# Kernel optimization log

Measured on AMD Instinct MI355X. Metric: run time of the kernel, lower is better.

## Reference

```python
import jax, jax.numpy as jnp
import numpy as np

ALPHA = 0.1  # leakyRNN default alpha


def setup_inputs() -> dict:
    key = jax.random.key(0)
    k1, k2, k3, k4 = jax.random.split(key, 4)
    B, T, N_in, n, N = 256, 2048, 3, 2, 128
    u = jax.random.normal(k1, (B, T, N_in), dtype=jnp.float32)
    matB = jax.random.uniform(k2, (N, N), dtype=jnp.float32)
    # scaled for recurrence stability over T=2048 steps (spectral radius of 0.9*I + 0.1*W < 1)
    wIn = jax.random.normal(k3, (n, N_in), dtype=jnp.float32) * 0.5
    wRec = jax.random.normal(k4, (n, n), dtype=jnp.float32) * 0.5
    return {"u": u, "matB": matB, "wIn": wIn, "wRec": wRec}


def reference(u, matB, wIn, wRec):
    B, T, _ = u.shape
    n = wRec.shape[0]
    N = matB.shape[0]

    # (bias=False, init_state_train=False -> y0 = 0)
    y0 = jnp.zeros((B, n), dtype=u.dtype)

    def step(y, xt):
        y = (1.0 - ALPHA) * y + ALPHA * (jax.nn.relu(y) @ wRec.T + xt @ wIn.T)
        return y, y

    _, hidden = jax.lax.scan(step, y0, jnp.swapaxes(u, 0, 1))  # [T,B,n]
    hidden = jnp.swapaxes(hidden, 0, 1)  # [B,T,n]

    # ZeroPad1d((0, N-n)) pads the last (feature) dim on the right
    x_padded = jnp.pad(hidden, ((0, 0), (0, 0), (0, N - n)))  # [B,T,N]

    # Orthonormal (Cayley) parametrization: A = B - B^T; Q solves Q @ (I+A) = (I-A)
    A = matB - matB.T
    I = jnp.eye(N, dtype=matB.dtype)
    Q = jnp.linalg.solve((I + A).T, (I - A).T).T  # (I-A) @ inv(I+A)

    # nn.Linear(N, N, bias=False) with weight Q: y = x @ Q^T
    return x_padded @ Q.T
```

## Files before the change

### kernel.cpp

```cpp
#include <hip/hip_runtime.h>

#define TT 2048
#define BATCH 256
#define LDC 132
#define NCOL 130

typedef float vfloat4 __attribute__((ext_vector_type(4)));


__global__ __launch_bounds__(256) void proj_kernel(
    const float* __restrict__ u, const float* __restrict__ wIn, float* __restrict__ ws)
{
    __shared__ float2 tile[64][33];
    const int tid = threadIdx.x;
    const int tb = blockIdx.x & 31;
    const int bb = blockIdx.x >> 5;
    const int t0 = tb * 64;
    const int b0 = bb * 32;

    const float w00 = 0.1f * wIn[0], w01 = 0.1f * wIn[1], w02 = 0.1f * wIn[2];
    const float w10 = 0.1f * wIn[3], w11 = 0.1f * wIn[4], w12 = 0.1f * wIn[5];

    const int tl  = tid & 63;
    const int bl0 = tid >> 6;
#pragma unroll
    for (int s = 0; s < 8; ++s) {
        int bl = bl0 + s * 4;
        const float* p = u + ((size_t)(b0 + bl) * TT + t0 + tl) * 3;
        float x = p[0], y = p[1], z = p[2];
        float2 dv;
        dv.x = fmaf(x, w00, fmaf(y, w01, z * w02));
        dv.y = fmaf(x, w10, fmaf(y, w11, z * w12));
        tile[tl][bl] = dv;
    }
    __syncthreads();

    float* d = ws + 256;
    const int bw  = tid & 31;
    const int tw0 = tid >> 5;
#pragma unroll
    for (int s = 0; s < 8; ++s) {
        int tw = tw0 + s * 8;
        *(float2*)(d + ((size_t)(t0 + tw) * BATCH + b0 + bw) * 2) = tile[tw][bw];
    }
}

__global__ __launch_bounds__(256) void ge_rnn_kernel(
    const float* __restrict__ matB, const float* __restrict__ wRec,
    float* __restrict__ ws)
{
    if (blockIdx.x == 0) {
        __shared__ __align__(16) float Mc[NCOL * LDC];
        __shared__ __align__(16) float fb[128];
        __shared__ float vb[256];
        const int tid = threadIdx.x;

        for (int e = tid; e < 128 * 128; e += 256) {
            int i = e >> 7, j = e & 127;
            float a = matB[i * 128 + j] - matB[j * 128 + i];
            Mc[j * LDC + i] = a + ((i == j) ? 1.0f : 0.0f);
        }
        for (int i = tid; i < 128; i += 256) {
            Mc[128 * LDC + i] = (i == 0) ? 1.0f : 0.0f;
            Mc[129 * LDC + i] = (i == 1) ? 1.0f : 0.0f;
        }
        __syncthreads();

        for (int k = 0; k < 127; ++k) {
            if (tid > k && tid < 128)
                fb[tid] = Mc[k * LDC + tid] / Mc[k * LDC + k];
            __syncthreads();
            int j = tid;
            if (j > k && j < NCOL) {
                float mkj = Mc[j * LDC + k];
                int i = k + 1;
                int iv = (i + 3) & ~3;
                if (iv > 128) iv = 128;
                for (; i < iv; ++i)
                    Mc[j * LDC + i] = fmaf(-fb[i], mkj, Mc[j * LDC + i]);
                for (; i < 128; i += 4) {
                    float4 m = *(float4*)&Mc[j * LDC + i];
                    float4 f = *(const float4*)&fb[i];
                    m.x = fmaf(-f.x, mkj, m.x);
                    m.y = fmaf(-f.y, mkj, m.y);
                    m.z = fmaf(-f.z, mkj, m.z);
                    m.w = fmaf(-f.w, mkj, m.w);
                    *(float4*)&Mc[j * LDC + i] = m;
                }
            }
            __syncthreads();
        }

        float r0 = 0.f, r1 = 0.f;
        if (tid < 128) {
            r0 = Mc[128 * LDC + tid];
            r1 = Mc[129 * LDC + tid];
        }
        for (int k = 127; k >= 0; --k) {
            if (tid == k) {
                float piv = Mc[k * LDC + k];
                vb[k]       = r0 / piv;
                vb[128 + k] = r1 / piv;
            }
            __syncthreads();
            if (tid < k) {
                float uik = Mc[k * LDC + tid];
                r0 = fmaf(-uik, vb[k],       r0);
                r1 = fmaf(-uik, vb[128 + k], r1);
            }
        }
        __syncthreads();

        if (tid < 128) {
            int i = tid;
            float q0 = vb[i], q1 = vb[128 + i];
            for (int j = 0; j < 128; ++j) {
                float aij = matB[i * 128 + j] - matB[j * 128 + i];
                q0 = fmaf(-aij, vb[j],       q0);
                q1 = fmaf(-aij, vb[128 + j], q1);
            }
            ws[i]       = q0;
            ws[128 + i] = q1;
        }
    } else if (blockIdx.x == 1) {
        const int b = threadIdx.x;
        float* dh = ws + 256;
        const float a00 = 0.1f * wRec[0], a01 = 0.1f * wRec[1];
        const float a10 = 0.1f * wRec[2], a11 = 0.1f * wRec[3];
        float y0 = 0.f, y1 = 0.f;

        const int G = 16;
        float2 cur[G], nxt[G];
#pragma unroll
        for (int k = 0; k < G; ++k)
            cur[k] = *(float2*)(dh + ((size_t)k * BATCH + b) * 2);

        for (int g = 0; g < TT / G; ++g) {
            if (g + 1 < TT / G) {
                int tn = (g + 1) * G;
#pragma unroll
                for (int k = 0; k < G; ++k)
                    nxt[k] = *(float2*)(dh + ((size_t)(tn + k) * BATCH + b) * 2);
            }
#pragma unroll
            for (int k = 0; k < G; ++k) {
                float rr0 = fmaxf(y0, 0.f), rr1 = fmaxf(y1, 0.f);
                float n0 = fmaf(rr0, a00, fmaf(rr1, a01, cur[k].x));
                float n1 = fmaf(rr0, a10, fmaf(rr1, a11, cur[k].y));
                y0 = fmaf(0.9f, y0, n0);
                y1 = fmaf(0.9f, y1, n1);
                cur[k].x = y0;
                cur[k].y = y1;
            }
#pragma unroll
            for (int k = 0; k < G; ++k)
                *(float2*)(dh + ((size_t)(g * G + k) * BATCH + b) * 2) = cur[k];
#pragma unroll
            for (int k = 0; k < G; ++k) cur[k] = nxt[k];
        }
    }
}

__global__ __launch_bounds__(256) void out_kernel(
    const float* __restrict__ ws, float* __restrict__ out)
{
    const int tid = threadIdx.x;
    const int jg  = tid & 31;
    const int sub = tid >> 5;
    float4 qa = *(const float4*)(ws + jg * 4);
    float4 qb = *(const float4*)(ws + 128 + jg * 4);
    const float* h = ws + 256;
    const int ngroups = BATCH * (TT / 8);
    for (int g = blockIdx.x; g < ngroups; g += gridDim.x) {
        int b = g >> 8;
        int t = (g & 255) * 8 + sub;
        float2 hv = *(const float2*)(h + ((size_t)t * BATCH + b) * 2);
        vfloat4 o;
        o.x = fmaf(hv.x, qa.x, hv.y * qb.x);
        o.y = fmaf(hv.x, qa.y, hv.y * qb.y);
        o.z = fmaf(hv.x, qa.z, hv.y * qb.z);
        o.w = fmaf(hv.x, qa.w, hv.y * qb.w);
        __builtin_nontemporal_store(o, (vfloat4*)(out + ((size_t)b * TT + t) * 128 + jg * 4));
    }
}

extern "C" void kernel_launch(void* const* d_in, const int* in_sizes, int n_in,
                              void* d_out, int out_size, void* d_ws, size_t ws_size,
                              hipStream_t stream) {
    const float* u    = (const float*)d_in[0];
    const float* matB = (const float*)d_in[1];
    const float* wIn  = (const float*)d_in[2];
    const float* wRec = (const float*)d_in[3];
    float* out = (float*)d_out;
    float* ws  = (float*)d_ws;

    hipLaunchKernelGGL(proj_kernel,   dim3(256),  dim3(256), 0, stream, u, wIn, ws);
    hipLaunchKernelGGL(ge_rnn_kernel, dim3(2),    dim3(256), 0, stream, matB, wRec, ws);
    hipLaunchKernelGGL(out_kernel,    dim3(8192), dim3(256), 0, stream, ws, out);
}
```

Before: 503.2 us.

## Split RNN across four blocks with t4-interleaved layout, L2 prefetch waves, and faster GE

Changes the workspace layout so each batch element owns a contiguous 8-float record per group of four timesteps. The recurrence now runs on four blocks of 64 lanes instead of one block of 256, with 16-byte loads in a double-buffered load/compute/store schedule. Three spare wavefronts per block read the block's slice ahead of time so it sits in cache. The Gaussian elimination also drops one barrier per pivot by computing the scale inline, and its back substitution now runs in a single wave using shuffles instead of barriers. The risk is the extra prefetch traffic and the added index arithmetic in out_kernel.

```diff
diff --git a/kernel.cpp b/kernel.cpp
--- a/kernel.cpp
+++ b/kernel.cpp
@@ -37,11 +37,20 @@
 
     float* d = ws + 256;
     const int bw  = tid & 31;
-    const int tw0 = tid >> 5;
-#pragma unroll
-    for (int s = 0; s < 8; ++s) {
-        int tw = tw0 + s * 8;
-        *(float2*)(d + ((size_t)(t0 + tw) * BATCH + b0 + bw) * 2) = tile[tw][bw];
+    const int tg0 = tid >> 5;
+#pragma unroll
+    for (int s = 0; s < 2; ++s) {
+        int t4l = tg0 + s * 8;
+        float2 a0 = tile[t4l * 4 + 0][bw];
+        float2 a1 = tile[t4l * 4 + 1][bw];
+        float2 a2 = tile[t4l * 4 + 2][bw];
+        float2 a3 = tile[t4l * 4 + 3][bw];
+        float* p = d + ((size_t)((t0 >> 2) + t4l) * BATCH + (b0 + bw)) * 8;
+        vfloat4 w0, w1;
+        w0.x = a0.x; w0.y = a0.y; w0.z = a1.x; w0.w = a1.y;
+        w1.x = a2.x; w1.y = a2.y; w1.z = a3.x; w1.w = a3.y;
+        *(vfloat4*)p       = w0;
+        *(vfloat4*)(p + 4) = w1;
     }
 }
 
@@ -51,7 +60,6 @@
 {
     if (blockIdx.x == 0) {
         __shared__ __align__(16) float Mc[NCOL * LDC];
-        __shared__ __align__(16) float fb[128];
         __shared__ float vb[256];
         const int tid = threadIdx.x;
 
@@ -67,46 +75,42 @@
         __syncthreads();
 
         for (int k = 0; k < 127; ++k) {
-            if (tid > k && tid < 128)
-                fb[tid] = Mc[k * LDC + tid] / Mc[k * LDC + k];
-            __syncthreads();
             int j = tid;
             if (j > k && j < NCOL) {
-                float mkj = Mc[j * LDC + k];
+                float scale = Mc[j * LDC + k] / Mc[k * LDC + k];
                 int i = k + 1;
                 int iv = (i + 3) & ~3;
                 if (iv > 128) iv = 128;
                 for (; i < iv; ++i)
-                    Mc[j * LDC + i] = fmaf(-fb[i], mkj, Mc[j * LDC + i]);
+                    Mc[j * LDC + i] = fmaf(-Mc[k * LDC + i], scale, Mc[j * LDC + i]);
                 for (; i < 128; i += 4) {
                     float4 m = *(float4*)&Mc[j * LDC + i];
-                    float4 f = *(const float4*)&fb[i];
-                    m.x = fmaf(-f.x, mkj, m.x);
-                    m.y = fmaf(-f.y, mkj, m.y);
-                    m.z = fmaf(-f.z, mkj, m.z);
-                    m.w = fmaf(-f.w, mkj, m.w);
+                    float4 f = *(const float4*)&Mc[k * LDC + i];
+                    m.x = fmaf(-f.x, scale, m.x);
+                    m.y = fmaf(-f.y, scale, m.y);
+                    m.z = fmaf(-f.z, scale, m.z);
+                    m.w = fmaf(-f.w, scale, m.w);
                     *(float4*)&Mc[j * LDC + i] = m;
                 }
             }
             __syncthreads();
         }
 
-        float r0 = 0.f, r1 = 0.f;
-        if (tid < 128) {
-            r0 = Mc[128 * LDC + tid];
-            r1 = Mc[129 * LDC + tid];
-        }
-        for (int k = 127; k >= 0; --k) {
-            if (tid == k) {
-                float piv = Mc[k * LDC + k];
-                vb[k]       = r0 / piv;
-                vb[128 + k] = r1 / piv;
-            }
-            __syncthreads();
-            if (tid < k) {
-                float uik = Mc[k * LDC + tid];
-                r0 = fmaf(-uik, vb[k],       r0);
-                r1 = fmaf(-uik, vb[128 + k], r1);
+        if (tid < 64) {
+            const int l = tid;
+            float r0 = Mc[128 * LDC + l],      s0 = Mc[129 * LDC + l];
+            float r1 = Mc[128 * LDC + l + 64], s1 = Mc[129 * LDC + l + 64];
+            for (int k = 127; k >= 0; --k) {
+                float Ukk = Mc[k * LDC + k];
+                float c0 = (k >= 64) ? r1 : r0;
+                float c1 = (k >= 64) ? s1 : s0;
+                float v0 = __shfl(c0, k & 63) / Ukk;
+                float v1 = __shfl(c1, k & 63) / Ukk;
+                if (l == (k & 63)) { vb[k] = v0; vb[128 + k] = v1; }
+                float ul = Mc[k * LDC + l];
+                float uh = Mc[k * LDC + l + 64];
+                if (l < k)      { r0 = fmaf(-ul, v0, r0); s0 = fmaf(-ul, v1, s0); }
+                if (l + 64 < k) { r1 = fmaf(-uh, v0, r1); s1 = fmaf(-uh, v1, s1); }
             }
         }
         __syncthreads();
@@ -122,42 +126,70 @@
             ws[i]       = q0;
             ws[128 + i] = q1;
         }
-    } else if (blockIdx.x == 1) {
-        const int b = threadIdx.x;
-        float* dh = ws + 256;
+    } else {
+        const int lane = threadIdx.x;
+        if (lane >= 64) {
+            const int pid = lane - 64;
+            const float* dd = ws + 256;
+            const size_t boff = (size_t)(blockIdx.x - 1) * 64 * 8;
+            float acc = 0.f;
+            for (int c = pid; c < 512 * 128; c += 192) {
+                int t4 = c >> 7, part = c & 127;
+                vfloat4 v = *(const vfloat4*)(dd + (size_t)t4 * (BATCH * 8) + boff + part * 4);
+                acc += v.x + v.y + v.z + v.w;
+            }
+            asm volatile("" :: "v"(acc));
+            return;
+        }
+        const int b = (blockIdx.x - 1) * 64 + lane;
+        float* base = ws + 256 + (size_t)b * 8;
         const float a00 = 0.1f * wRec[0], a01 = 0.1f * wRec[1];
         const float a10 = 0.1f * wRec[2], a11 = 0.1f * wRec[3];
         float y0 = 0.f, y1 = 0.f;
 
-        const int G = 16;
-        float2 cur[G], nxt[G];
-#pragma unroll
-        for (int k = 0; k < G; ++k)
-            cur[k] = *(float2*)(dh + ((size_t)k * BATCH + b) * 2);
-
-        for (int g = 0; g < TT / G; ++g) {
-            if (g + 1 < TT / G) {
-                int tn = (g + 1) * G;
-#pragma unroll
-                for (int k = 0; k < G; ++k)
-                    nxt[k] = *(float2*)(dh + ((size_t)(tn + k) * BATCH + b) * 2);
-            }
-#pragma unroll
-            for (int k = 0; k < G; ++k) {
-                float rr0 = fmaxf(y0, 0.f), rr1 = fmaxf(y1, 0.f);
-                float n0 = fmaf(rr0, a00, fmaf(rr1, a01, cur[k].x));
-                float n1 = fmaf(rr0, a10, fmaf(rr1, a11, cur[k].y));
-                y0 = fmaf(0.9f, y0, n0);
-                y1 = fmaf(0.9f, y1, n1);
-                cur[k].x = y0;
-                cur[k].y = y1;
-            }
-#pragma unroll
-            for (int k = 0; k < G; ++k)
-                *(float2*)(dh + ((size_t)(g * G + k) * BATCH + b) * 2) = cur[k];
-#pragma unroll
-            for (int k = 0; k < G; ++k) cur[k] = nxt[k];
-        }
+        vfloat4 A[16], Bv[16];
+
+#define RNN_STEP(d0, d1) do {                                   \
+        float rr0 = fmaxf(y0, 0.f), rr1 = fmaxf(y1, 0.f);       \
+        float p0 = fmaf(0.9f, y0, (d0));                        \
+        float p1 = fmaf(0.9f, y1, (d1));                        \
+        y0 = fmaf(rr1, a01, fmaf(rr0, a00, p0));                \
+        y1 = fmaf(rr1, a11, fmaf(rr0, a10, p1));                \
+        (d0) = y0; (d1) = y1; } while (0)
+
+        auto LOAD = [&](vfloat4* buf, int g) {
+#pragma unroll
+            for (int k = 0; k < 8; ++k) {
+                const float* p = base + (size_t)(g * 8 + k) * (BATCH * 8);
+                buf[2 * k]     = *(const vfloat4*)p;
+                buf[2 * k + 1] = *(const vfloat4*)(p + 4);
+            }
+        };
+        auto CSTORE = [&](vfloat4* buf, int g) {
+#pragma unroll
+            for (int k = 0; k < 8; ++k) {
+                vfloat4 v0 = buf[2 * k], v1 = buf[2 * k + 1];
+                RNN_STEP(v0.x, v0.y);
+                RNN_STEP(v0.z, v0.w);
+                RNN_STEP(v1.x, v1.y);
+                RNN_STEP(v1.z, v1.w);
+                float* p = base + (size_t)(g * 8 + k) * (BATCH * 8);
+                *(vfloat4*)p       = v0;
+                *(vfloat4*)(p + 4) = v1;
+            }
+        };
+
+        LOAD(A, 0);
+        for (int g = 0; g < 62; g += 2) {
+            LOAD(Bv, g + 1);
+            CSTORE(A, g);
+            LOAD(A, g + 2);
+            CSTORE(Bv, g + 1);
+        }
+        LOAD(Bv, 63);
+        CSTORE(A, 62);
+        CSTORE(Bv, 63);
+#undef RNN_STEP
     }
 }
 
@@ -174,7 +206,8 @@
     for (int g = blockIdx.x; g < ngroups; g += gridDim.x) {
         int b = g >> 8;
         int t = (g & 255) * 8 + sub;
-        float2 hv = *(const float2*)(h + ((size_t)t * BATCH + b) * 2);
+        const float* hp = h + ((size_t)(t >> 2) * BATCH + b) * 8 + (t & 3) * 2;
+        float2 hv = *(const float2*)hp;
         vfloat4 o;
         o.x = fmaf(hv.x, qa.x, hv.y * qb.x);
         o.y = fmaf(hv.x, qa.y, hv.y * qb.y);
@@ -195,6 +228,6 @@
     float* ws  = (float*)d_ws;
 
     hipLaunchKernelGGL(proj_kernel,   dim3(256),  dim3(256), 0, stream, u, wIn, ws);
-    hipLaunchKernelGGL(ge_rnn_kernel, dim3(2),    dim3(256), 0, stream, matB, wRec, ws);
+    hipLaunchKernelGGL(ge_rnn_kernel, dim3(5),    dim3(256), 0, stream, matB, wRec, ws);
     hipLaunchKernelGGL(out_kernel,    dim3(8192), dim3(256), 0, stream, ws, out);
 }
```

Result: slower. 542.2 us (+7.7%).
